# Optimization experiments

Measured on AMD Instinct MI355X. Metric: run time of the kernel, lower is better.

## Reference

```python
import jax, jax.numpy as jnp
import numpy as np

OUT = 7  # output_size of AdaptiveMaxPool2d


def _roi_pool(images, rois, roi_idx):
    # images: [N,C,H,W]; rois: [R,4] rel coords (x1,y1,x2,y2); roi_idx: [R]
    n, c, h, w = images.shape
    x1 = jnp.floor(rois[:, 0] * w).astype(jnp.int32)
    y1 = jnp.floor(rois[:, 1] * h).astype(jnp.int32)
    x2 = jnp.ceil(rois[:, 2] * w).astype(jnp.int32)
    y2 = jnp.ceil(rois[:, 3] * h).astype(jnp.int32)
    Hr = y2 - y1  # per-ROI crop height
    Wr = x2 - x1  # per-ROI crop width

    feats = images[roi_idx]  # [R,C,H,W] gather per-ROI source image
    hh = jnp.arange(h)
    ww = jnp.arange(w)
    neg = jnp.finfo(images.dtype).min

    # Adaptive max pool is separable: max over row-bins, then col-bins.
    # PyTorch adaptive bins over a region of size L: [floor(i*L/OUT), ceil((i+1)*L/OUT))
    rows = []
    for i in range(OUT):  # small fixed loop over output rows
        s = y1 + (i * Hr) // OUT
        e = y1 + ((i + 1) * Hr + OUT - 1) // OUT  # ceil
        m = (hh[None, :] >= s[:, None]) & (hh[None, :] < e[:, None])  # [R,H]
        rows.append(jnp.max(jnp.where(m[:, None, :, None], feats, neg), axis=2))  # [R,C,W]
    rowp = jnp.stack(rows, axis=2)  # [R,C,OUT,W]

    cols = []
    for j in range(OUT):  # small fixed loop over output cols
        s = x1 + (j * Wr) // OUT
        e = x1 + ((j + 1) * Wr + OUT - 1) // OUT
        m = (ww[None, :] >= s[:, None]) & (ww[None, :] < e[:, None])  # [R,W]
        cols.append(jnp.max(jnp.where(m[:, None, None, :], rowp, neg), axis=3))  # [R,C,OUT]
    return jnp.stack(cols, axis=3)  # [R,C,OUT,OUT]


def setup_inputs() -> dict:
    key = jax.random.key(0)
    k1, k2, k3 = jax.random.split(key, 3)
    N, C, H, W, R = 8, 256, 56, 56, 256
    images = jax.random.normal(k1, (N, C, H, W), dtype=jnp.float32)
    # build valid boxes: x1<x2, y1<y2 in [0,1]
    pts = jax.random.uniform(k2, (R, 2, 2), dtype=jnp.float32)
    lo = jnp.min(pts, axis=1)
    hi = jnp.max(pts, axis=1)
    rois = jnp.stack([lo[:, 0], lo[:, 1], hi[:, 0], hi[:, 1]], axis=1)  # [R,4]
    roi_idx = jax.random.randint(k3, (R,), 0, N)
    return {"images": images, "rois": rois, "roi_idx": roi_idx}


def reference(images, rois, roi_idx):
    return _roi_pool(images, rois, roi_idx)
```

## Files before the change

### kernel.cpp

```cpp
#include <hip/hip_runtime.h>

#define OUTS 7
#define CC 256
#define HH 56
#define WW 56
#define PX (HH * WW)
#define STRIDE 57
#define SPLIT 2
#define MAXROI 96

__global__ __launch_bounds__(256) void roipool_kernel(
    const float* __restrict__ images, const float* __restrict__ rois,
    const int* __restrict__ roi_idx, float* __restrict__ out, int R)
{
    __shared__ float4 plane4[STRIDE * HH];
    __shared__ int    list[MAXROI];
    __shared__ unsigned short ys[MAXROI * 7];
    __shared__ unsigned short xs[MAXROI * 7];
    __shared__ int cnt;

    const int b  = blockIdx.x;
    const int s  = b & (SPLIT - 1);
    const int pq = b >> 1;
    const int n  = pq >> 6;
    const int c0 = (pq & 63) * 4;
    const int t  = threadIdx.x;

    if (t < 64) {
        int base = 0;
        #pragma unroll
        for (int k = 0; k < 4; ++k) {
            int r = k * 64 + t;
            bool match = (r < R) && (roi_idx[r] == n);
            unsigned long long mask = __ballot(match);
            int pos = base + __popcll(mask & ((1ULL << t) - 1ULL));
            if (match && pos < MAXROI) list[pos] = r;
            base += __popcll(mask);
        }
        if (t == 0) cnt = (base < MAXROI) ? base : MAXROI;
    }

    const float* base0 = images + (size_t)(n * CC + c0) * PX;
    #pragma unroll
    for (int k = 0; k < 4; ++k) {
        int idx = t + k * 256;
        if (idx < PX / 4) {
            float4 a = reinterpret_cast<const float4*>(base0)[idx];
            float4 bb = reinterpret_cast<const float4*>(base0 + PX)[idx];
            float4 cc = reinterpret_cast<const float4*>(base0 + 2 * PX)[idx];
            float4 dd = reinterpret_cast<const float4*>(base0 + 3 * PX)[idx];
            int y  = idx / 14;
            int x0 = (idx - y * 14) * 4;
            float4* dst = &plane4[y * STRIDE + x0];
            dst[0] = make_float4(a.x, bb.x, cc.x, dd.x);
            dst[1] = make_float4(a.y, bb.y, cc.y, dd.y);
            dst[2] = make_float4(a.z, bb.z, cc.z, dd.z);
            dst[3] = make_float4(a.w, bb.w, cc.w, dd.w);
        }
    }
    __syncthreads();

    const int count = cnt;

    for (int e = t; e < count * 7; e += 256) {
        int m = e / 7, i = e - m * 7;
        int r = list[m];
        float4 rv = reinterpret_cast<const float4*>(rois)[r];
        int x1 = (int)floorf(rv.x * (float)WW);
        int y1 = (int)floorf(rv.y * (float)HH);
        int x2 = (int)ceilf (rv.z * (float)WW);
        int y2 = (int)ceilf (rv.w * (float)HH);
        int Hr = y2 - y1, Wr = x2 - x1;
        int sy = y1 + (i * Hr) / 7, ey = y1 + ((i + 1) * Hr + 6) / 7;
        int sx = x1 + (i * Wr) / 7, ex = x1 + ((i + 1) * Wr + 6) / 7;
        ys[m * 7 + i] = (unsigned short)(sy | (ey << 8));
        xs[m * 7 + i] = (unsigned short)(sx | (ex << 8));
    }
    __syncthreads();

    const int wv   = t >> 6;
    const int lane = t & 63;
    const int i = lane / 7;
    const int j = lane - i * 7;

    if (lane < OUTS * OUTS) {
        for (int m = (wv << 1) + s; m < count; m += SPLIT * 4) {
            int r = list[m];
            int yse = ys[m * 7 + i];
            int xse = xs[m * 7 + j];
            int sy = yse & 255, ey = yse >> 8;
            int sx = xse & 255, ex = xse >> 8;

            float a0 = -3.402823466e+38f;
            float a1 = a0, a2 = a0, a3 = a0;
            const float4* rowp = &plane4[sy * STRIDE];
            for (int y = sy; y < ey; ++y, rowp += STRIDE) {
                for (int x = sx; x < ex; ++x) {
                    float4 v = rowp[x];
                    a0 = fmaxf(a0, v.x);
                    a1 = fmaxf(a1, v.y);
                    a2 = fmaxf(a2, v.z);
                    a3 = fmaxf(a3, v.w);
                }
            }
            size_t o = ((size_t)r * CC + c0) * (OUTS * OUTS) + lane;
            out[o]       = a0;
            out[o + 49]  = a1;
            out[o + 98]  = a2;
            out[o + 147] = a3;
        }
    }
}

extern "C" void kernel_launch(void* const* d_in, const int* in_sizes, int n_in,
                              void* d_out, int out_size, void* d_ws, size_t ws_size,
                              hipStream_t stream) {
    const float* images  = (const float*)d_in[0];
    const float* rois    = (const float*)d_in[1];
    const int*   roi_idx = (const int*)d_in[2];
    float* out = (float*)d_out;

    int R = in_sizes[2];
    int N = in_sizes[0] / (CC * HH * WW);

    int grid = N * (CC / 4) * SPLIT;
    roipool_kernel<<<grid, 256, 0, stream>>>(images, rois, roi_idx, out, R);
}
```

Baseline: 99.16 us.

## Pack two channels per block and unroll bin max loop with clamped indices

Each block now stages two channels, interleaved as float2 in shared memory, instead of four, which doubles the grid and halves LDS use per block so more blocks can be resident. The inner pooling loop is unrolled to two rows by four columns, with indices clamped to the bin edge so duplicate reads stay correct for max. This raises parallelism and instruction-level parallelism in the max reduction. In exchange, each ROI's bins are recomputed twice as often, ROI list building is repeated across twice as many blocks, and clamped duplicate loads waste LDS bandwidth on small bins.

```diff
diff --git a/kernel.cpp b/kernel.cpp
--- a/kernel.cpp
+++ b/kernel.cpp
@@ -5,7 +5,7 @@
 #define HH 56
 #define WW 56
 #define PX (HH * WW)
-#define STRIDE 57
+#define STRIDE 58
 #define SPLIT 2
 #define MAXROI 96
 
@@ -13,7 +13,7 @@
     const float* __restrict__ images, const float* __restrict__ rois,
     const int* __restrict__ roi_idx, float* __restrict__ out, int R)
 {
-    __shared__ float4 plane4[STRIDE * HH];
+    __shared__ __align__(16) float2 plane2[STRIDE * HH];
     __shared__ int    list[MAXROI];
     __shared__ unsigned short ys[MAXROI * 7];
     __shared__ unsigned short xs[MAXROI * 7];
@@ -21,9 +21,9 @@
 
     const int b  = blockIdx.x;
     const int s  = b & (SPLIT - 1);
-    const int pq = b >> 1;
-    const int n  = pq >> 6;
-    const int c0 = (pq & 63) * 4;
+    const int pp = b >> 1;
+    const int n  = pp >> 7;
+    const int c0 = (pp & 127) * 2;
     const int t  = threadIdx.x;
 
     if (t < 64) {
@@ -40,22 +40,19 @@
         if (t == 0) cnt = (base < MAXROI) ? base : MAXROI;
     }
 
-    const float* base0 = images + (size_t)(n * CC + c0) * PX;
+    const float4* srcA = reinterpret_cast<const float4*>(images + (size_t)(n * CC + c0)     * PX);
+    const float4* srcB = reinterpret_cast<const float4*>(images + (size_t)(n * CC + c0 + 1) * PX);
     #pragma unroll
     for (int k = 0; k < 4; ++k) {
         int idx = t + k * 256;
         if (idx < PX / 4) {
-            float4 a = reinterpret_cast<const float4*>(base0)[idx];
-            float4 bb = reinterpret_cast<const float4*>(base0 + PX)[idx];
-            float4 cc = reinterpret_cast<const float4*>(base0 + 2 * PX)[idx];
-            float4 dd = reinterpret_cast<const float4*>(base0 + 3 * PX)[idx];
+            float4 a  = srcA[idx];
+            float4 bb = srcB[idx];
             int y  = idx / 14;
             int x0 = (idx - y * 14) * 4;
-            float4* dst = &plane4[y * STRIDE + x0];
-            dst[0] = make_float4(a.x, bb.x, cc.x, dd.x);
-            dst[1] = make_float4(a.y, bb.y, cc.y, dd.y);
-            dst[2] = make_float4(a.z, bb.z, cc.z, dd.z);
-            dst[3] = make_float4(a.w, bb.w, cc.w, dd.w);
+            float4* dst = reinterpret_cast<float4*>(&plane2[y * STRIDE + x0]);
+            dst[0] = make_float4(a.x, bb.x, a.y, bb.y);
+            dst[1] = make_float4(a.z, bb.z, a.w, bb.w);
         }
     }
     __syncthreads();
@@ -91,23 +88,27 @@
             int sy = yse & 255, ey = yse >> 8;
             int sx = xse & 255, ex = xse >> 8;
 
-            float a0 = -3.402823466e+38f;
-            float a1 = a0, a2 = a0, a3 = a0;
-            const float4* rowp = &plane4[sy * STRIDE];
-            for (int y = sy; y < ey; ++y, rowp += STRIDE) {
-                for (int x = sx; x < ex; ++x) {
-                    float4 v = rowp[x];
-                    a0 = fmaxf(a0, v.x);
-                    a1 = fmaxf(a1, v.y);
-                    a2 = fmaxf(a2, v.z);
-                    a3 = fmaxf(a3, v.w);
+            const float nf = -3.402823466e+38f;
+            float a0 = nf, a1 = nf;
+
+            for (int y = sy; y < ey; y += 2) {
+                const float2* r0 = plane2 + y * STRIDE;
+                const float2* r1 = plane2 + min(y + 1, ey - 1) * STRIDE;
+                for (int x = sx; x < ex; x += 4) {
+                    int xb = min(x + 1, ex - 1);
+                    int xc = min(x + 2, ex - 1);
+                    int xd = min(x + 3, ex - 1);
+                    float2 v0 = r0[x],  v1 = r0[xb], v2 = r0[xc], v3 = r0[xd];
+                    float2 w0 = r1[x],  w1 = r1[xb], w2 = r1[xc], w3 = r1[xd];
+                    a0 = fmaxf(a0, fmaxf(fmaxf(fmaxf(v0.x, v1.x), fmaxf(v2.x, v3.x)),
+                                         fmaxf(fmaxf(w0.x, w1.x), fmaxf(w2.x, w3.x))));
+                    a1 = fmaxf(a1, fmaxf(fmaxf(fmaxf(v0.y, v1.y), fmaxf(v2.y, v3.y)),
+                                         fmaxf(fmaxf(w0.y, w1.y), fmaxf(w2.y, w3.y))));
                 }
             }
             size_t o = ((size_t)r * CC + c0) * (OUTS * OUTS) + lane;
-            out[o]       = a0;
-            out[o + 49]  = a1;
-            out[o + 98]  = a2;
-            out[o + 147] = a3;
+            out[o]      = a0;
+            out[o + 49] = a1;
         }
     }
 }
@@ -123,6 +124,6 @@
     int R = in_sizes[2];
     int N = in_sizes[0] / (CC * HH * WW);
 
-    int grid = N * (CC / 4) * SPLIT;
+    int grid = N * (CC / 2) * SPLIT;
     roipool_kernel<<<grid, 256, 0, stream>>>(images, rois, roi_idx, out, R);
 }
```

Measured after the change: 90.25 us. 1.1x faster.
